# Performance work log

Hardware: AMD Instinct MI355X
Metric: run time of the kernel (lower is better)

The kernel has to match this reference:

```python
import jax, jax.numpy as jnp
import numpy as np
from jax import lax

SEQ_LEN = 4096
INPUT_SIZE = 1024
HIDDEN = 1024
NUM_CLASSES = 3


def setup_inputs() -> dict:
    key = jax.random.key(0)
    ks = jax.random.split(key, 12)
    s = 1.0 / np.sqrt(HIDDEN)  # torch LSTM/Linear uniform init scale
    def u(k, shape):
        return jax.random.uniform(k, shape, jnp.float32, -s, s)
    inp = jax.random.normal(ks[0], (SEQ_LEN, 1, INPUT_SIZE), jnp.float32)
    return {
        "inp": inp,
        # forward-direction LSTM params (gate order i,f,g,o as in torch)
        "Wih_f": u(ks[1], (4 * HIDDEN, INPUT_SIZE)),
        "Whh_f": u(ks[2], (4 * HIDDEN, HIDDEN)),
        "bih_f": u(ks[3], (4 * HIDDEN,)),
        "bhh_f": u(ks[4], (4 * HIDDEN,)),
        # backward-direction LSTM params
        "Wih_b": u(ks[5], (4 * HIDDEN, INPUT_SIZE)),
        "Whh_b": u(ks[6], (4 * HIDDEN, HIDDEN)),
        "bih_b": u(ks[7], (4 * HIDDEN,)),
        "bhh_b": u(ks[8], (4 * HIDDEN,)),
        # output head: Linear(2*HIDDEN, 3)
        "W_ho": u(ks[9], (NUM_CLASSES, 2 * HIDDEN)),
        "b_ho": u(ks[10], (NUM_CLASSES,)),
    }


def _lstm_last_h(x, Wih, Whh, bih, bhh):
    # x: (T, B, I) -> final hidden state (B, H)
    H = Whh.shape[1]
    B = x.shape[1]
    bias = bih + bhh
    # precompute input projections for all timesteps: (T, B, 4H)
    xg = jnp.einsum('tbi,gi->tbg', x, Wih) + bias

    def step(carry, xt):
        h, c = carry
        gates = xt + h @ Whh.T  # (B, 4H)
        i, f, g, o = jnp.split(gates, 4, axis=-1)
        c = jax.nn.sigmoid(f) * c + jax.nn.sigmoid(i) * jnp.tanh(g)
        h = jax.nn.sigmoid(o) * jnp.tanh(c)
        return (h, c), None

    init = (jnp.zeros((B, H), x.dtype), jnp.zeros((B, H), x.dtype))
    (hT, _), _ = lax.scan(step, init, xg)
    return hT


def reference(inp, Wih_f, Whh_f, bih_f, bhh_f, Wih_b, Whh_b, bih_b, bhh_b, W_ho, b_ho):
    h_fwd = _lstm_last_h(inp, Wih_f, Whh_f, bih_f, bhh_f)          # (1, H)
    h_bwd = _lstm_last_h(inp[::-1], Wih_b, Whh_b, bih_b, bhh_b)    # (1, H)
    hidden = jnp.concatenate([h_fwd, h_bwd], axis=-1)              # (1, 2H)
    # Dropout(p=0.35) is identity in eval mode.
    return hidden @ W_ho.T + b_ho                                  # (1, 3)
```

## Files before the change

kernel.cpp:

```cpp
#include <hip/hip_runtime.h>
#include <stdint.h>
#include <math.h>


#define T_SEQ 4096
#define ISZ   1024
#define HID   1024
#define NB_DIR 128
#define NB_TOT 256
#define NTHR   512
#define ROWS_PER_BLK 32
#define UNITS_PER_BLK 8
#define KW 64
#define PAD_CHUNK 68

typedef unsigned long long u64;

__device__ __forceinline__ float fast_sigmoid(float x) {
    return 1.0f / (1.0f + __expf(-x));
}
__device__ __forceinline__ float fast_tanh(float x) {
    return 1.0f - 2.0f / (__expf(2.0f * x) + 1.0f);
}

__global__ __launch_bounds__(NTHR, 2)
void bilstm_persistent(const float* __restrict__ x,
                       const float* __restrict__ Wih_f, const float* __restrict__ Whh_f,
                       const float* __restrict__ bih_f, const float* __restrict__ bhh_f,
                       const float* __restrict__ Wih_b, const float* __restrict__ Whh_b,
                       const float* __restrict__ bih_b, const float* __restrict__ bhh_b,
                       u64* hpack )
{
    const int tid = threadIdx.x;
    const int blk = blockIdx.x;
    const int dir = blk >> 7;
    const int lb  = blk & 127;
    const int u0  = lb * UNITS_PER_BLK;
    const int r_local = tid >> 4;
    const int kc  = tid & 15;
    const int q   = r_local >> 3;
    const int uu  = r_local & 7;
    const int grow = q * HID + u0 + uu;

    const float* Wih = dir ? Wih_b : Wih_f;
    const float* Whh = dir ? Whh_b : Whh_f;
    const float* bih = dir ? bih_b : bih_f;
    const float* bhh = dir ? bhh_b : bhh_f;

    u64* hp = hpack + (size_t)dir * 2 * HID;

    __shared__ float lds_h[16 * PAD_CHUNK];
    __shared__ float lds_x[16 * PAD_CHUNK];
    __shared__ float lds_g[ROWS_PER_BLK];
    __shared__ float lds_bias[ROWS_PER_BLK];

    float wih[KW], whh[KW];
    {
        const float* pih = Wih + (size_t)grow * ISZ + kc * KW;
        const float* phh = Whh + (size_t)grow * HID + kc * KW;
        #pragma unroll
        for (int j = 0; j < KW; j += 4) {
            float4 a = *(const float4*)(pih + j);
            wih[j] = a.x; wih[j+1] = a.y; wih[j+2] = a.z; wih[j+3] = a.w;
            float4 b4 = *(const float4*)(phh + j);
            whh[j] = b4.x; whh[j+1] = b4.y; whh[j+2] = b4.z; whh[j+3] = b4.w;
        }
    }
    #pragma unroll
    for (int j = 0; j < KW; ++j) {
        asm volatile("" : "+v"(wih[j]));
        asm volatile("" : "+v"(whh[j]));
    }

    if (tid < ROWS_PER_BLK) {
        int qq = tid >> 3, u2 = tid & 7;
        int gr = qq * HID + u0 + u2;
        lds_bias[tid] = bih[gr] + bhh[gr];
    }

    float c_state = 0.0f;

    {
        int xrow = dir ? (T_SEQ - 1) : 0;
        const float* xp = x + (size_t)xrow * ISZ;
        int i0 = tid * 2;
        float2 v = *(const float2*)(xp + i0);
        *(float2*)&lds_x[(i0 >> 6) * PAD_CHUNK + (i0 & 63)] = v;
    }
    __syncthreads();
    float xacc = 0.0f;
    {
        const float* lx = lds_x + kc * PAD_CHUNK;
        #pragma unroll
        for (int j = 0; j < KW; j += 4) {
            float4 v = *(const float4*)(lx + j);
            xacc += wih[j]*v.x + wih[j+1]*v.y + wih[j+2]*v.z + wih[j+3]*v.w;
        }
    }

    bool dead = false;

    for (int t = 0; t < T_SEQ; ++t) {
        float pre = xacc;

        if (t > 0) {
            u64* src = hp + ((size_t)((t - 1) & 1)) * HID;
            const int pi = tid * 2;
            u64 e0 = 0, e1 = 0;
            if (!dead) {
                int sp = 0;
                while (((e0 = __hip_atomic_load(src + pi, __ATOMIC_RELAXED,
                                                __HIP_MEMORY_SCOPE_AGENT)) >> 32)
                       != (unsigned)t) {
                    if (++sp > (1 << 21)) { dead = true; break; }
                }
                sp = 0;
                if (!dead) {
                    while (((e1 = __hip_atomic_load(src + pi + 1, __ATOMIC_RELAXED,
                                                    __HIP_MEMORY_SCOPE_AGENT)) >> 32)
                           != (unsigned)t) {
                        if (++sp > (1 << 21)) { dead = true; break; }
                    }
                }
            }
            lds_h[(pi >> 6) * PAD_CHUNK + (pi & 63)] =
                __uint_as_float((unsigned)(e0 & 0xffffffffu));
            lds_h[((pi + 1) >> 6) * PAD_CHUNK + ((pi + 1) & 63)] =
                __uint_as_float((unsigned)(e1 & 0xffffffffu));
            __syncthreads();
            const float* lh = lds_h + kc * PAD_CHUNK;
            #pragma unroll
            for (int j = 0; j < KW; j += 4) {
                float4 v = *(const float4*)(lh + j);
                pre += whh[j]*v.x + whh[j+1]*v.y + whh[j+2]*v.z + whh[j+3]*v.w;
            }
        }

        pre += __shfl_xor(pre, 1);
        pre += __shfl_xor(pre, 2);
        pre += __shfl_xor(pre, 4);
        pre += __shfl_xor(pre, 8);
        if (kc == 0) lds_g[r_local] = pre + lds_bias[r_local];
        __syncthreads();

        if (tid < UNITS_PER_BLK) {
            float gi = lds_g[0 * 8 + tid];
            float gf = lds_g[1 * 8 + tid];
            float gg = lds_g[2 * 8 + tid];
            float go = lds_g[3 * 8 + tid];
            float si = fast_sigmoid(gi);
            float sf = fast_sigmoid(gf);
            float so = fast_sigmoid(go);
            float tg = fast_tanh(gg);
            c_state = sf * c_state + si * tg;
            float hval = so * fast_tanh(c_state);
            u64 pk = ((u64)(unsigned)(t + 1) << 32) | (u64)__float_as_uint(hval);
            __hip_atomic_store(hp + ((size_t)(t & 1)) * HID + u0 + tid, pk,
                               __ATOMIC_RELAXED, __HIP_MEMORY_SCOPE_AGENT);
        }

        if (t + 1 < T_SEQ) {
            int xrow = dir ? (T_SEQ - 2 - t) : (t + 1);
            const float* xp = x + (size_t)xrow * ISZ;
            int i0 = tid * 2;
            float2 v = *(const float2*)(xp + i0);
            *(float2*)&lds_x[(i0 >> 6) * PAD_CHUNK + (i0 & 63)] = v;
            __syncthreads();
            xacc = 0.0f;
            const float* lx = lds_x + kc * PAD_CHUNK;
            #pragma unroll
            for (int j = 0; j < KW; j += 4) {
                float4 v4 = *(const float4*)(lx + j);
                xacc += wih[j]*v4.x + wih[j+1]*v4.y + wih[j+2]*v4.z + wih[j+3]*v4.w;
            }
        }
    }
}

__global__ void head_kernel(const float* __restrict__ W_ho,
                            const float* __restrict__ b_ho,
                            const u64* __restrict__ hpack,
                            float* __restrict__ out)
{
    const u64* hf  = hpack + 1 * HID;
    const u64* hbk = hpack + 2 * HID + 1 * HID;
    __shared__ float r0[4], r1[4], r2[4];
    int tid = threadIdx.x;
    float p0 = 0.f, p1 = 0.f, p2 = 0.f;
    for (int i = tid; i < 2 * HID; i += 256) {
        u64 e = (i < HID) ? hf[i] : hbk[i - HID];
        float hv = __uint_as_float((unsigned)(e & 0xffffffffu));
        p0 += W_ho[0 * 2 * HID + i] * hv;
        p1 += W_ho[1 * 2 * HID + i] * hv;
        p2 += W_ho[2 * 2 * HID + i] * hv;
    }
    #pragma unroll
    for (int m = 1; m < 64; m <<= 1) {
        p0 += __shfl_xor(p0, m);
        p1 += __shfl_xor(p1, m);
        p2 += __shfl_xor(p2, m);
    }
    int w = tid >> 6;
    if ((tid & 63) == 0) { r0[w] = p0; r1[w] = p1; r2[w] = p2; }
    __syncthreads();
    if (tid == 0) {
        out[0] = b_ho[0] + r0[0] + r0[1] + r0[2] + r0[3];
        out[1] = b_ho[1] + r1[0] + r1[1] + r1[2] + r1[3];
        out[2] = b_ho[2] + r2[0] + r2[1] + r2[2] + r2[3];
    }
}

extern "C" void kernel_launch(void* const* d_in, const int* in_sizes, int n_in,
                              void* d_out, int out_size, void* d_ws, size_t ws_size,
                              hipStream_t stream) {
    const float* x     = (const float*)d_in[0];
    const float* Wih_f = (const float*)d_in[1];
    const float* Whh_f = (const float*)d_in[2];
    const float* bih_f = (const float*)d_in[3];
    const float* bhh_f = (const float*)d_in[4];
    const float* Wih_b = (const float*)d_in[5];
    const float* Whh_b = (const float*)d_in[6];
    const float* bih_b = (const float*)d_in[7];
    const float* bhh_b = (const float*)d_in[8];
    const float* W_ho  = (const float*)d_in[9];
    const float* b_ho  = (const float*)d_in[10];

    u64* hpack = (u64*)d_ws;

    hipMemsetAsync(d_ws, 0, 2 * 2 * HID * sizeof(u64), stream);

    bilstm_persistent<<<NB_TOT, NTHR, 0, stream>>>(
        x, Wih_f, Whh_f, bih_f, bhh_f, Wih_b, Whh_b, bih_b, bhh_b, hpack);

    head_kernel<<<1, 256, 0, stream>>>(W_ho, b_ho, hpack, (float*)d_out);
}
```

Measured before the change: 8.955 ms.

## Hoist input projection into a separate GEMM and slim the recurrent step

Computes the input projections for all timesteps and both directions up front with a tiled FP32 GEMM into workspace, as the reference does, so the persistent recurrent kernel keeps only Whh in registers. Each wavefront now owns one hidden unit, and the four gates are gathered with lane shuffles instead of an LDS round trip. This drops one __syncthreads per step, and the LDS h buffer is double-buffered. The cost is an extra 128MB workspace buffer plus the write and reread traffic for it. The old fused kernel is kept as a fallback when the workspace is too small.

```diff
diff --git a/kernel.cpp b/kernel.cpp
--- a/kernel.cpp
+++ b/kernel.cpp
@@ -1,18 +1,15 @@
 #include <hip/hip_runtime.h>
 #include <stdint.h>
-#include <math.h>
 
 
 #define T_SEQ 4096
 #define ISZ   1024
 #define HID   1024
+#define G4H   4096
 #define NB_DIR 128
 #define NB_TOT 256
-#define NTHR   512
-#define ROWS_PER_BLK 32
-#define UNITS_PER_BLK 8
-#define KW 64
-#define PAD_CHUNK 68
+#define NTHR  512
+#define PAD   68
 
 typedef unsigned long long u64;
 
@@ -23,88 +20,124 @@
     return 1.0f - 2.0f / (__expf(2.0f * x) + 1.0f);
 }
 
+#define GM 64
+#define GN 64
+#define GK 32
+
+__global__ __launch_bounds__(256)
+void xproj_gemm(const float* __restrict__ x,
+                const float* __restrict__ Wih_f, const float* __restrict__ bih_f,
+                const float* __restrict__ bhh_f,
+                const float* __restrict__ Wih_b, const float* __restrict__ bih_b,
+                const float* __restrict__ bhh_b,
+                float* __restrict__ xg)
+{
+    const int dir = blockIdx.z;
+    const float* Wih = dir ? Wih_b : Wih_f;
+    const float* bih = dir ? bih_b : bih_f;
+    const float* bhh = dir ? bhh_b : bhh_f;
+    const int m0 = blockIdx.y * GM;
+    const int n0 = blockIdx.x * GN;
+    const int tid = threadIdx.x;
+    const int ms = tid >> 2;
+    const int kq = tid & 3;
+    const int tm = tid >> 4;
+    const int tn = tid & 15;
+
+    __shared__ float As[GK][GM + 4];
+    __shared__ float Bs[GK][GN + 4];
+
+    float acc[4][4] = {};
+
+    const int mrow = m0 + ms;
+    const int xrow = dir ? (T_SEQ - 1 - mrow) : mrow;
+    const float* ap = x + (size_t)xrow * ISZ + kq * 8;
+    const float* bp = Wih + (size_t)(n0 + ms) * ISZ + kq * 8;
+
+    for (int k0 = 0; k0 < ISZ; k0 += GK) {
+        float4 a0 = *(const float4*)(ap + k0);
+        float4 a1 = *(const float4*)(ap + k0 + 4);
+        float4 b0 = *(const float4*)(bp + k0);
+        float4 b1 = *(const float4*)(bp + k0 + 4);
+        __syncthreads();
+        const int kb = kq * 8;
+        As[kb+0][ms]=a0.x; As[kb+1][ms]=a0.y; As[kb+2][ms]=a0.z; As[kb+3][ms]=a0.w;
+        As[kb+4][ms]=a1.x; As[kb+5][ms]=a1.y; As[kb+6][ms]=a1.z; As[kb+7][ms]=a1.w;
+        Bs[kb+0][ms]=b0.x; Bs[kb+1][ms]=b0.y; Bs[kb+2][ms]=b0.z; Bs[kb+3][ms]=b0.w;
+        Bs[kb+4][ms]=b1.x; Bs[kb+5][ms]=b1.y; Bs[kb+6][ms]=b1.z; Bs[kb+7][ms]=b1.w;
+        __syncthreads();
+        #pragma unroll
+        for (int k = 0; k < GK; ++k) {
+            float4 av = *(const float4*)&As[k][tm * 4];
+            float4 bv = *(const float4*)&Bs[k][tn * 4];
+            acc[0][0] += av.x*bv.x; acc[0][1] += av.x*bv.y; acc[0][2] += av.x*bv.z; acc[0][3] += av.x*bv.w;
+            acc[1][0] += av.y*bv.x; acc[1][1] += av.y*bv.y; acc[1][2] += av.y*bv.z; acc[1][3] += av.y*bv.w;
+            acc[2][0] += av.z*bv.x; acc[2][1] += av.z*bv.y; acc[2][2] += av.z*bv.z; acc[2][3] += av.z*bv.w;
+            acc[3][0] += av.w*bv.x; acc[3][1] += av.w*bv.y; acc[3][2] += av.w*bv.z; acc[3][3] += av.w*bv.w;
+        }
+    }
+
+    const int gc = n0 + tn * 4;
+    float4 bb1 = *(const float4*)(bih + gc);
+    float4 bb2 = *(const float4*)(bhh + gc);
+    float bx = bb1.x + bb2.x, by = bb1.y + bb2.y, bz = bb1.z + bb2.z, bw = bb1.w + bb2.w;
+    float* op = xg + ((size_t)dir << 24) + (size_t)(m0 + tm * 4) * G4H + gc;
+    #pragma unroll
+    for (int i = 0; i < 4; ++i) {
+        float4 v;
+        v.x = acc[i][0] + bx; v.y = acc[i][1] + by;
+        v.z = acc[i][2] + bz; v.w = acc[i][3] + bw;
+        *(float4*)(op + (size_t)i * G4H) = v;
+    }
+}
+
 __global__ __launch_bounds__(NTHR, 2)
-void bilstm_persistent(const float* __restrict__ x,
-                       const float* __restrict__ Wih_f, const float* __restrict__ Whh_f,
-                       const float* __restrict__ bih_f, const float* __restrict__ bhh_f,
-                       const float* __restrict__ Wih_b, const float* __restrict__ Whh_b,
-                       const float* __restrict__ bih_b, const float* __restrict__ bhh_b,
-                       u64* hpack )
+void bilstm_rec(const float* __restrict__ xg,
+                const float* __restrict__ Whh_f, const float* __restrict__ Whh_b,
+                u64* hpack)
 {
     const int tid = threadIdx.x;
     const int blk = blockIdx.x;
     const int dir = blk >> 7;
     const int lb  = blk & 127;
-    const int u0  = lb * UNITS_PER_BLK;
-    const int r_local = tid >> 4;
-    const int kc  = tid & 15;
-    const int q   = r_local >> 3;
-    const int uu  = r_local & 7;
-    const int grow = q * HID + u0 + uu;
-
-    const float* Wih = dir ? Wih_b : Wih_f;
+    const int u0  = lb * 8;
+    const int w   = tid >> 6;
+    const int lane = tid & 63;
+    const int q   = lane >> 4;
+    const int kc  = lane & 15;
+    const int grow = q * HID + u0 + w;
+
     const float* Whh = dir ? Whh_b : Whh_f;
-    const float* bih = dir ? bih_b : bih_f;
-    const float* bhh = dir ? bhh_b : bhh_f;
-
+    const float* xgd = xg + ((size_t)dir << 24);
     u64* hp = hpack + (size_t)dir * 2 * HID;
 
-    __shared__ float lds_h[16 * PAD_CHUNK];
-    __shared__ float lds_x[16 * PAD_CHUNK];
-    __shared__ float lds_g[ROWS_PER_BLK];
-    __shared__ float lds_bias[ROWS_PER_BLK];
-
-    float wih[KW], whh[KW];
+    __shared__ float lds_h[2][16 * PAD];
+
+    float whh[64];
     {
-        const float* pih = Wih + (size_t)grow * ISZ + kc * KW;
-        const float* phh = Whh + (size_t)grow * HID + kc * KW;
+        const float* phh = Whh + (size_t)grow * HID + kc * 64;
         #pragma unroll
-        for (int j = 0; j < KW; j += 4) {
-            float4 a = *(const float4*)(pih + j);
-            wih[j] = a.x; wih[j+1] = a.y; wih[j+2] = a.z; wih[j+3] = a.w;
-            float4 b4 = *(const float4*)(phh + j);
-            whh[j] = b4.x; whh[j+1] = b4.y; whh[j+2] = b4.z; whh[j+3] = b4.w;
+        for (int j = 0; j < 64; j += 4) {
+            float4 v = *(const float4*)(phh + j);
+            whh[j] = v.x; whh[j+1] = v.y; whh[j+2] = v.z; whh[j+3] = v.w;
         }
     }
     #pragma unroll
-    for (int j = 0; j < KW; ++j) {
-        asm volatile("" : "+v"(wih[j]));
-        asm volatile("" : "+v"(whh[j]));
-    }
-
-    if (tid < ROWS_PER_BLK) {
-        int qq = tid >> 3, u2 = tid & 7;
-        int gr = qq * HID + u0 + u2;
-        lds_bias[tid] = bih[gr] + bhh[gr];
-    }
+    for (int j = 0; j < 64; ++j) asm volatile("" : "+v"(whh[j]));
 
     float c_state = 0.0f;
-
-    {
-        int xrow = dir ? (T_SEQ - 1) : 0;
-        const float* xp = x + (size_t)xrow * ISZ;
-        int i0 = tid * 2;
-        float2 v = *(const float2*)(xp + i0);
-        *(float2*)&lds_x[(i0 >> 6) * PAD_CHUNK + (i0 & 63)] = v;
-    }
-    __syncthreads();
-    float xacc = 0.0f;
-    {
-        const float* lx = lds_x + kc * PAD_CHUNK;
-        #pragma unroll
-        for (int j = 0; j < KW; j += 4) {
-            float4 v = *(const float4*)(lx + j);
-            xacc += wih[j]*v.x + wih[j+1]*v.y + wih[j+2]*v.z + wih[j+3]*v.w;
-        }
-    }
+    float xgv = 0.0f;
+    if (kc == 0) xgv = xgd[grow];
+    asm volatile("" : "+v"(xgv));
 
     bool dead = false;
 
     for (int t = 0; t < T_SEQ; ++t) {
-        float pre = xacc;
+        float pre = 0.0f;
 
         if (t > 0) {
-            u64* src = hp + ((size_t)((t - 1) & 1)) * HID;
+            const int b = (t - 1) & 1;
+            u64* src = hp + (size_t)b * HID;
             const int pi = tid * 2;
             u64 e0 = 0, e1 = 0;
             if (!dead) {
@@ -123,16 +156,16 @@
                     }
                 }
             }
-            lds_h[(pi >> 6) * PAD_CHUNK + (pi & 63)] =
-                __uint_as_float((unsigned)(e0 & 0xffffffffu));
-            lds_h[((pi + 1) >> 6) * PAD_CHUNK + ((pi + 1) & 63)] =
-                __uint_as_float((unsigned)(e1 & 0xffffffffu));
+            float2 hv;
+            hv.x = __uint_as_float((unsigned)(e0 & 0xffffffffu));
+            hv.y = __uint_as_float((unsigned)(e1 & 0xffffffffu));
+            *(float2*)&lds_h[b][(pi >> 6) * PAD + (pi & 63)] = hv;
             __syncthreads();
-            const float* lh = lds_h + kc * PAD_CHUNK;
+            const float* lh = &lds_h[b][kc * PAD];
             #pragma unroll
-            for (int j = 0; j < KW; j += 4) {
-                float4 v = *(const float4*)(lh + j);
-                pre += whh[j]*v.x + whh[j+1]*v.y + whh[j+2]*v.z + whh[j+3]*v.w;
+            for (int j = 0; j < 16; ++j) {
+                float4 v = *(const float4*)(lh + j * 4);
+                pre += whh[j*4+0]*v.x + whh[j*4+1]*v.y + whh[j*4+2]*v.z + whh[j*4+3]*v.w;
             }
         }
 
@@ -140,38 +173,29 @@
         pre += __shfl_xor(pre, 2);
         pre += __shfl_xor(pre, 4);
         pre += __shfl_xor(pre, 8);
-        if (kc == 0) lds_g[r_local] = pre + lds_bias[r_local];
-        __syncthreads();
-
-        if (tid < UNITS_PER_BLK) {
-            float gi = lds_g[0 * 8 + tid];
-            float gf = lds_g[1 * 8 + tid];
-            float gg = lds_g[2 * 8 + tid];
-            float go = lds_g[3 * 8 + tid];
-            float si = fast_sigmoid(gi);
-            float sf = fast_sigmoid(gf);
-            float so = fast_sigmoid(go);
-            float tg = fast_tanh(gg);
+
+        float pg = pre + xgv;
+
+        float pf_g = __shfl(pg, 16);
+        float pg_g = __shfl(pg, 32);
+        float po_g = __shfl(pg, 48);
+
+        if (lane == 0) {
+            float si = fast_sigmoid(pg);
+            float sf = fast_sigmoid(pf_g);
+            float tg = fast_tanh(pg_g);
+            float so = fast_sigmoid(po_g);
             c_state = sf * c_state + si * tg;
             float hval = so * fast_tanh(c_state);
             u64 pk = ((u64)(unsigned)(t + 1) << 32) | (u64)__float_as_uint(hval);
-            __hip_atomic_store(hp + ((size_t)(t & 1)) * HID + u0 + tid, pk,
+            __hip_atomic_store(hp + (size_t)(t & 1) * HID + u0 + w, pk,
                                __ATOMIC_RELAXED, __HIP_MEMORY_SCOPE_AGENT);
         }
 
         if (t + 1 < T_SEQ) {
-            int xrow = dir ? (T_SEQ - 2 - t) : (t + 1);
-            const float* xp = x + (size_t)xrow * ISZ;
-            int i0 = tid * 2;
-            float2 v = *(const float2*)(xp + i0);
-            *(float2*)&lds_x[(i0 >> 6) * PAD_CHUNK + (i0 & 63)] = v;
-            __syncthreads();
-            xacc = 0.0f;
-            const float* lx = lds_x + kc * PAD_CHUNK;
-            #pragma unroll
-            for (int j = 0; j < KW; j += 4) {
-                float4 v4 = *(const float4*)(lx + j);
-                xacc += wih[j]*v4.x + wih[j+1]*v4.y + wih[j+2]*v4.z + wih[j+3]*v4.w;
+            if (kc == 0) {
+                xgv = xgd[(size_t)(t + 1) * G4H + grow];
+                asm volatile("" : "+v"(xgv));
             }
         }
     }
@@ -210,6 +234,150 @@
     }
 }
 
+#define ROWS_PER_BLK 32
+#define UNITS_PER_BLK 8
+#define KW 64
+
+__global__ __launch_bounds__(NTHR, 2)
+void bilstm_fallback(const float* __restrict__ x,
+                     const float* __restrict__ Wih_f, const float* __restrict__ Whh_f,
+                     const float* __restrict__ bih_f, const float* __restrict__ bhh_f,
+                     const float* __restrict__ Wih_b, const float* __restrict__ Whh_b,
+                     const float* __restrict__ bih_b, const float* __restrict__ bhh_b,
+                     u64* hpack)
+{
+    const int tid = threadIdx.x;
+    const int blk = blockIdx.x;
+    const int dir = blk >> 7;
+    const int lb  = blk & 127;
+    const int u0  = lb * UNITS_PER_BLK;
+    const int r_local = tid >> 4;
+    const int kc  = tid & 15;
+    const int q   = r_local >> 3;
+    const int uu  = r_local & 7;
+    const int grow = q * HID + u0 + uu;
+
+    const float* Wih = dir ? Wih_b : Wih_f;
+    const float* Whh = dir ? Whh_b : Whh_f;
+    const float* bih = dir ? bih_b : bih_f;
+    const float* bhh = dir ? bhh_b : bhh_f;
+    u64* hp = hpack + (size_t)dir * 2 * HID;
+
+    __shared__ float lds_h[16 * PAD];
+    __shared__ float lds_x[16 * PAD];
+    __shared__ float lds_g[ROWS_PER_BLK];
+    __shared__ float lds_bias[ROWS_PER_BLK];
+
+    float wih[KW], whh[KW];
+    {
+        const float* pih = Wih + (size_t)grow * ISZ + kc * KW;
+        const float* phh = Whh + (size_t)grow * HID + kc * KW;
+        #pragma unroll
+        for (int j = 0; j < KW; j += 4) {
+            float4 a = *(const float4*)(pih + j);
+            wih[j] = a.x; wih[j+1] = a.y; wih[j+2] = a.z; wih[j+3] = a.w;
+            float4 b4 = *(const float4*)(phh + j);
+            whh[j] = b4.x; whh[j+1] = b4.y; whh[j+2] = b4.z; whh[j+3] = b4.w;
+        }
+    }
+    #pragma unroll
+    for (int j = 0; j < KW; ++j) {
+        asm volatile("" : "+v"(wih[j]));
+        asm volatile("" : "+v"(whh[j]));
+    }
+    if (tid < ROWS_PER_BLK) {
+        int qq = tid >> 3, u2 = tid & 7;
+        int gr = qq * HID + u0 + u2;
+        lds_bias[tid] = bih[gr] + bhh[gr];
+    }
+    float c_state = 0.0f;
+    {
+        int xrow = dir ? (T_SEQ - 1) : 0;
+        const float* xp = x + (size_t)xrow * ISZ;
+        int i0 = tid * 2;
+        float2 v = *(const float2*)(xp + i0);
+        *(float2*)&lds_x[(i0 >> 6) * PAD + (i0 & 63)] = v;
+    }
+    __syncthreads();
+    float xacc = 0.0f;
+    {
+        const float* lx = lds_x + kc * PAD;
+        #pragma unroll
+        for (int j = 0; j < KW; j += 4) {
+            float4 v = *(const float4*)(lx + j);
+            xacc += wih[j]*v.x + wih[j+1]*v.y + wih[j+2]*v.z + wih[j+3]*v.w;
+        }
+    }
+    bool dead = false;
+    for (int t = 0; t < T_SEQ; ++t) {
+        float pre = xacc;
+        if (t > 0) {
+            u64* src = hp + ((size_t)((t - 1) & 1)) * HID;
+            const int pi = tid * 2;
+            u64 e0 = 0, e1 = 0;
+            if (!dead) {
+                int sp = 0;
+                while (((e0 = __hip_atomic_load(src + pi, __ATOMIC_RELAXED,
+                                                __HIP_MEMORY_SCOPE_AGENT)) >> 32) != (unsigned)t) {
+                    if (++sp > (1 << 21)) { dead = true; break; }
+                }
+                sp = 0;
+                if (!dead) {
+                    while (((e1 = __hip_atomic_load(src + pi + 1, __ATOMIC_RELAXED,
+                                                    __HIP_MEMORY_SCOPE_AGENT)) >> 32) != (unsigned)t) {
+                        if (++sp > (1 << 21)) { dead = true; break; }
+                    }
+                }
+            }
+            lds_h[(pi >> 6) * PAD + (pi & 63)] = __uint_as_float((unsigned)(e0 & 0xffffffffu));
+            lds_h[((pi + 1) >> 6) * PAD + ((pi + 1) & 63)] = __uint_as_float((unsigned)(e1 & 0xffffffffu));
+            __syncthreads();
+            const float* lh = lds_h + kc * PAD;
+            #pragma unroll
+            for (int j = 0; j < KW; j += 4) {
+                float4 v = *(const float4*)(lh + j);
+                pre += whh[j]*v.x + whh[j+1]*v.y + whh[j+2]*v.z + whh[j+3]*v.w;
+            }
+        }
+        pre += __shfl_xor(pre, 1);
+        pre += __shfl_xor(pre, 2);
+        pre += __shfl_xor(pre, 4);
+        pre += __shfl_xor(pre, 8);
+        if (kc == 0) lds_g[r_local] = pre + lds_bias[r_local];
+        __syncthreads();
+        if (tid < UNITS_PER_BLK) {
+            float gi = lds_g[0 * 8 + tid];
+            float gf = lds_g[1 * 8 + tid];
+            float gg = lds_g[2 * 8 + tid];
+            float go = lds_g[3 * 8 + tid];
+            float si = fast_sigmoid(gi);
+            float sf = fast_sigmoid(gf);
+            float so = fast_sigmoid(go);
+            float tg = fast_tanh(gg);
+            c_state = sf * c_state + si * tg;
+            float hval = so * fast_tanh(c_state);
+            u64 pk = ((u64)(unsigned)(t + 1) << 32) | (u64)__float_as_uint(hval);
+            __hip_atomic_store(hp + ((size_t)(t & 1)) * HID + u0 + tid, pk,
+                               __ATOMIC_RELAXED, __HIP_MEMORY_SCOPE_AGENT);
+        }
+        if (t + 1 < T_SEQ) {
+            int xrow = dir ? (T_SEQ - 2 - t) : (t + 1);
+            const float* xp = x + (size_t)xrow * ISZ;
+            int i0 = tid * 2;
+            float2 v = *(const float2*)(xp + i0);
+            *(float2*)&lds_x[(i0 >> 6) * PAD + (i0 & 63)] = v;
+            __syncthreads();
+            xacc = 0.0f;
+            const float* lx = lds_x + kc * PAD;
+            #pragma unroll
+            for (int j = 0; j < KW; j += 4) {
+                float4 v4 = *(const float4*)(lx + j);
+                xacc += wih[j]*v4.x + wih[j+1]*v4.y + wih[j+2]*v4.z + wih[j+3]*v4.w;
+            }
+        }
+    }
+}
+
 extern "C" void kernel_launch(void* const* d_in, const int* in_sizes, int n_in,
                               void* d_out, int out_size, void* d_ws, size_t ws_size,
                               hipStream_t stream) {
@@ -226,11 +394,19 @@
     const float* b_ho  = (const float*)d_in[10];
 
     u64* hpack = (u64*)d_ws;
+    float* xg = (float*)((char*)d_ws + 32768);
+    const size_t need = 32768 + (size_t)2 * T_SEQ * G4H * sizeof(float);
 
     hipMemsetAsync(d_ws, 0, 2 * 2 * HID * sizeof(u64), stream);
 
-    bilstm_persistent<<<NB_TOT, NTHR, 0, stream>>>(
-        x, Wih_f, Whh_f, bih_f, bhh_f, Wih_b, Whh_b, bih_b, bhh_b, hpack);
-
+    if (ws_size >= need) {
+        dim3 gg(G4H / GN, T_SEQ / GM, 2);
+        xproj_gemm<<<gg, 256, 0, stream>>>(x, Wih_f, bih_f, bhh_f,
+                                           Wih_b, bih_b, bhh_b, xg);
+        bilstm_rec<<<NB_TOT, NTHR, 0, stream>>>(xg, Whh_f, Whh_b, hpack);
+    } else {
+        bilstm_fallback<<<NB_TOT, NTHR, 0, stream>>>(
+            x, Wih_f, Whh_f, bih_f, bhh_f, Wih_b, Whh_b, bih_b, bhh_b, hpack);
+    }
     head_kernel<<<1, 256, 0, stream>>>(W_ho, b_ho, hpack, (float*)d_out);
 }
```

Result: faster. 8.397 ms (-6.2%).

## Precompute input projections with a separate GEMM and simplify recurrent step

Applied to the files above, without the earlier changes.

Moves the per-step input projection out of the persistent recurrent kernel into a tiled FP32 GEMM that writes the gate preactivations plus bias for all timesteps to workspace. The recurrent kernel then keeps only the Whh slice in registers, gives each wavefront one hidden unit with all four gates, and reduces with wave shuffles instead of an LDS gate buffer and an extra barrier. It also double-buffers the h vector in LDS with an XOR swizzle, removing the per-step x load and second syncthreads from the serial path. In exchange it adds a large workspace (128 MB of xg) and a GEMM launch before the recurrence.

```diff
diff --git a/kernel.cpp b/kernel.cpp
--- a/kernel.cpp
+++ b/kernel.cpp
@@ -1,18 +1,12 @@
 #include <hip/hip_runtime.h>
 #include <stdint.h>
-#include <math.h>
 
 
 #define T_SEQ 4096
 #define ISZ   1024
 #define HID   1024
-#define NB_DIR 128
 #define NB_TOT 256
-#define NTHR   512
-#define ROWS_PER_BLK 32
-#define UNITS_PER_BLK 8
-#define KW 64
-#define PAD_CHUNK 68
+#define NTHR  512
 
 typedef unsigned long long u64;
 
@@ -23,156 +17,199 @@
     return 1.0f - 2.0f / (__expf(2.0f * x) + 1.0f);
 }
 
+#define PIN4(v) asm volatile("" : "+v"(v.x), "+v"(v.y), "+v"(v.z), "+v"(v.w))
+#define DOT4(a, b) ((a).x*(b).x + (a).y*(b).y + (a).z*(b).z + (a).w*(b).w)
+
+#define GM 64
+#define GN 64
+#define GK 32
+
+__global__ __launch_bounds__(256)
+void xproj_gemm(const float* __restrict__ x,
+                const float* __restrict__ Wih_f, const float* __restrict__ bih_f,
+                const float* __restrict__ bhh_f,
+                const float* __restrict__ Wih_b, const float* __restrict__ bih_b,
+                const float* __restrict__ bhh_b,
+                float* __restrict__ xg)
+{
+    const int dir = blockIdx.z;
+    const float* Wih = dir ? Wih_b : Wih_f;
+    const float* bih = dir ? bih_b : bih_f;
+    const float* bhh = dir ? bhh_b : bhh_f;
+    const int m0 = blockIdx.y * GM;
+    const int n0 = blockIdx.x * GN;
+    const int tid = threadIdx.x;
+    const int ms = tid >> 2;
+    const int kq = tid & 3;
+    const int tm = tid >> 4;
+    const int tn = tid & 15;
+
+    __shared__ float As[GK][GM + 4];
+    __shared__ float Bs[GK][GN + 4];
+
+    float acc[4][4] = {};
+
+    const int mrow = m0 + ms;
+    const int xrow = dir ? (T_SEQ - 1 - mrow) : mrow;
+    const float* ap = x + (size_t)xrow * ISZ + kq * 8;
+    const float* bp = Wih + (size_t)(n0 + ms) * ISZ + kq * 8;
+
+    for (int k0 = 0; k0 < ISZ; k0 += GK) {
+        float4 a0 = *(const float4*)(ap + k0);
+        float4 a1 = *(const float4*)(ap + k0 + 4);
+        float4 b0 = *(const float4*)(bp + k0);
+        float4 b1 = *(const float4*)(bp + k0 + 4);
+        __syncthreads();
+        const int kb = kq * 8;
+        As[kb+0][ms]=a0.x; As[kb+1][ms]=a0.y; As[kb+2][ms]=a0.z; As[kb+3][ms]=a0.w;
+        As[kb+4][ms]=a1.x; As[kb+5][ms]=a1.y; As[kb+6][ms]=a1.z; As[kb+7][ms]=a1.w;
+        Bs[kb+0][ms]=b0.x; Bs[kb+1][ms]=b0.y; Bs[kb+2][ms]=b0.z; Bs[kb+3][ms]=b0.w;
+        Bs[kb+4][ms]=b1.x; Bs[kb+5][ms]=b1.y; Bs[kb+6][ms]=b1.z; Bs[kb+7][ms]=b1.w;
+        __syncthreads();
+        #pragma unroll
+        for (int k = 0; k < GK; ++k) {
+            float4 av = *(const float4*)&As[k][tm * 4];
+            float4 bv = *(const float4*)&Bs[k][tn * 4];
+            acc[0][0] += av.x*bv.x; acc[0][1] += av.x*bv.y; acc[0][2] += av.x*bv.z; acc[0][3] += av.x*bv.w;
+            acc[1][0] += av.y*bv.x; acc[1][1] += av.y*bv.y; acc[1][2] += av.y*bv.z; acc[1][3] += av.y*bv.w;
+            acc[2][0] += av.z*bv.x; acc[2][1] += av.z*bv.y; acc[2][2] += av.z*bv.z; acc[2][3] += av.z*bv.w;
+            acc[3][0] += av.w*bv.x; acc[3][1] += av.w*bv.y; acc[3][2] += av.w*bv.z; acc[3][3] += av.w*bv.w;
+        }
+    }
+
+    const int gc = n0 + tn * 4;
+    float4 bb1 = *(const float4*)(bih + gc);
+    float4 bb2 = *(const float4*)(bhh + gc);
+    float bx = bb1.x + bb2.x, by = bb1.y + bb2.y, bz = bb1.z + bb2.z, bw = bb1.w + bb2.w;
+    float* op = xg + ((size_t)dir << 24) + (size_t)(m0 + tm * 4) * 4096 + gc;
+    #pragma unroll
+    for (int i = 0; i < 4; ++i) {
+        float4 v;
+        v.x = acc[i][0] + bx; v.y = acc[i][1] + by;
+        v.z = acc[i][2] + bz; v.w = acc[i][3] + bw;
+        *(float4*)(op + (size_t)i * 4096) = v;
+    }
+}
+
 __global__ __launch_bounds__(NTHR, 2)
-void bilstm_persistent(const float* __restrict__ x,
-                       const float* __restrict__ Wih_f, const float* __restrict__ Whh_f,
-                       const float* __restrict__ bih_f, const float* __restrict__ bhh_f,
-                       const float* __restrict__ Wih_b, const float* __restrict__ Whh_b,
-                       const float* __restrict__ bih_b, const float* __restrict__ bhh_b,
-                       u64* hpack )
+void bilstm_rec(const float* __restrict__ xg,
+                const float* __restrict__ Whh_f, const float* __restrict__ Whh_b,
+                u64* hpack)
 {
     const int tid = threadIdx.x;
     const int blk = blockIdx.x;
     const int dir = blk >> 7;
     const int lb  = blk & 127;
-    const int u0  = lb * UNITS_PER_BLK;
-    const int r_local = tid >> 4;
-    const int kc  = tid & 15;
-    const int q   = r_local >> 3;
-    const int uu  = r_local & 7;
-    const int grow = q * HID + u0 + uu;
-
-    const float* Wih = dir ? Wih_b : Wih_f;
+    const int u0  = lb * 8;
+    const int w   = tid >> 6;
+    const int l   = tid & 63;
+    const int unit = u0 + w;
+    const int xsh = ((l >> 1) & 3) << 2;
+
     const float* Whh = dir ? Whh_b : Whh_f;
-    const float* bih = dir ? bih_b : bih_f;
-    const float* bhh = dir ? bhh_b : bhh_f;
-
+    const float* xgd = xg + ((size_t)dir << 24);
     u64* hp = hpack + (size_t)dir * 2 * HID;
 
-    __shared__ float lds_h[16 * PAD_CHUNK];
-    __shared__ float lds_x[16 * PAD_CHUNK];
-    __shared__ float lds_g[ROWS_PER_BLK];
-    __shared__ float lds_bias[ROWS_PER_BLK];
-
-    float wih[KW], whh[KW];
-    {
-        const float* pih = Wih + (size_t)grow * ISZ + kc * KW;
-        const float* phh = Whh + (size_t)grow * HID + kc * KW;
-        #pragma unroll
-        for (int j = 0; j < KW; j += 4) {
-            float4 a = *(const float4*)(pih + j);
-            wih[j] = a.x; wih[j+1] = a.y; wih[j+2] = a.z; wih[j+3] = a.w;
-            float4 b4 = *(const float4*)(phh + j);
-            whh[j] = b4.x; whh[j+1] = b4.y; whh[j+2] = b4.z; whh[j+3] = b4.w;
-        }
-    }
-    #pragma unroll
-    for (int j = 0; j < KW; ++j) {
-        asm volatile("" : "+v"(wih[j]));
-        asm volatile("" : "+v"(whh[j]));
-    }
-
-    if (tid < ROWS_PER_BLK) {
-        int qq = tid >> 3, u2 = tid & 7;
-        int gr = qq * HID + u0 + u2;
-        lds_bias[tid] = bih[gr] + bhh[gr];
-    }
+    __shared__ __align__(16) float lds_h[2][HID];
+
+    const float* wp0 = Whh + (size_t)(0 * HID + unit) * HID + l * 16;
+    const float* wp1 = Whh + (size_t)(1 * HID + unit) * HID + l * 16;
+    const float* wp2 = Whh + (size_t)(2 * HID + unit) * HID + l * 16;
+    const float* wp3 = Whh + (size_t)(3 * HID + unit) * HID + l * 16;
+    float4 w00 = *(const float4*)(wp0 + 0),  w01 = *(const float4*)(wp0 + 4);
+    float4 w02 = *(const float4*)(wp0 + 8),  w03 = *(const float4*)(wp0 + 12);
+    float4 w10 = *(const float4*)(wp1 + 0),  w11 = *(const float4*)(wp1 + 4);
+    float4 w12 = *(const float4*)(wp1 + 8),  w13 = *(const float4*)(wp1 + 12);
+    float4 w20 = *(const float4*)(wp2 + 0),  w21 = *(const float4*)(wp2 + 4);
+    float4 w22 = *(const float4*)(wp2 + 8),  w23 = *(const float4*)(wp2 + 12);
+    float4 w30 = *(const float4*)(wp3 + 0),  w31 = *(const float4*)(wp3 + 4);
+    float4 w32 = *(const float4*)(wp3 + 8),  w33 = *(const float4*)(wp3 + 12);
+    PIN4(w00); PIN4(w01); PIN4(w02); PIN4(w03);
+    PIN4(w10); PIN4(w11); PIN4(w12); PIN4(w13);
+    PIN4(w20); PIN4(w21); PIN4(w22); PIN4(w23);
+    PIN4(w30); PIN4(w31); PIN4(w32); PIN4(w33);
 
     float c_state = 0.0f;
-
-    {
-        int xrow = dir ? (T_SEQ - 1) : 0;
-        const float* xp = x + (size_t)xrow * ISZ;
-        int i0 = tid * 2;
-        float2 v = *(const float2*)(xp + i0);
-        *(float2*)&lds_x[(i0 >> 6) * PAD_CHUNK + (i0 & 63)] = v;
-    }
-    __syncthreads();
-    float xacc = 0.0f;
-    {
-        const float* lx = lds_x + kc * PAD_CHUNK;
-        #pragma unroll
-        for (int j = 0; j < KW; j += 4) {
-            float4 v = *(const float4*)(lx + j);
-            xacc += wih[j]*v.x + wih[j+1]*v.y + wih[j+2]*v.z + wih[j+3]*v.w;
-        }
-    }
+    float xgv = 0.0f;
+    if (l < 4) xgv = xgd[(size_t)l * HID + unit];
+    asm volatile("" : "+v"(xgv));
 
     bool dead = false;
 
     for (int t = 0; t < T_SEQ; ++t) {
-        float pre = xacc;
+        float s0 = 0.f, s1 = 0.f, s2 = 0.f, s3 = 0.f;
 
         if (t > 0) {
-            u64* src = hp + ((size_t)((t - 1) & 1)) * HID;
-            const int pi = tid * 2;
+            const int b = (t - 1) & 1;
+            u64* src = hp + (size_t)b * HID;
+            const int k0 = tid * 2;
             u64 e0 = 0, e1 = 0;
             if (!dead) {
                 int sp = 0;
-                while (((e0 = __hip_atomic_load(src + pi, __ATOMIC_RELAXED,
+                while (((e0 = __hip_atomic_load(src + k0, __ATOMIC_RELAXED,
                                                 __HIP_MEMORY_SCOPE_AGENT)) >> 32)
                        != (unsigned)t) {
                     if (++sp > (1 << 21)) { dead = true; break; }
                 }
                 sp = 0;
                 if (!dead) {
-                    while (((e1 = __hip_atomic_load(src + pi + 1, __ATOMIC_RELAXED,
+                    while (((e1 = __hip_atomic_load(src + k0 + 1, __ATOMIC_RELAXED,
                                                     __HIP_MEMORY_SCOPE_AGENT)) >> 32)
                            != (unsigned)t) {
                         if (++sp > (1 << 21)) { dead = true; break; }
                     }
                 }
             }
-            lds_h[(pi >> 6) * PAD_CHUNK + (pi & 63)] =
-                __uint_as_float((unsigned)(e0 & 0xffffffffu));
-            lds_h[((pi + 1) >> 6) * PAD_CHUNK + ((pi + 1) & 63)] =
-                __uint_as_float((unsigned)(e1 & 0xffffffffu));
+            const int mi = (k0 & ~15) | ((k0 & 15) ^ (((k0 >> 5) & 3) << 2));
+            float2 hv;
+            hv.x = __uint_as_float((unsigned)(e0 & 0xffffffffu));
+            hv.y = __uint_as_float((unsigned)(e1 & 0xffffffffu));
+            *(float2*)&lds_h[b][mi] = hv;
             __syncthreads();
-            const float* lh = lds_h + kc * PAD_CHUNK;
-            #pragma unroll
-            for (int j = 0; j < KW; j += 4) {
-                float4 v = *(const float4*)(lh + j);
-                pre += whh[j]*v.x + whh[j+1]*v.y + whh[j+2]*v.z + whh[j+3]*v.w;
-            }
-        }
-
-        pre += __shfl_xor(pre, 1);
-        pre += __shfl_xor(pre, 2);
-        pre += __shfl_xor(pre, 4);
-        pre += __shfl_xor(pre, 8);
-        if (kc == 0) lds_g[r_local] = pre + lds_bias[r_local];
-        __syncthreads();
-
-        if (tid < UNITS_PER_BLK) {
-            float gi = lds_g[0 * 8 + tid];
-            float gf = lds_g[1 * 8 + tid];
-            float gg = lds_g[2 * 8 + tid];
-            float go = lds_g[3 * 8 + tid];
+
+            const float* lh = &lds_h[b][l * 16];
+            float4 h0 = *(const float4*)(lh + (0  ^ xsh));
+            float4 h1 = *(const float4*)(lh + (4  ^ xsh));
+            float4 h2 = *(const float4*)(lh + (8  ^ xsh));
+            float4 h3 = *(const float4*)(lh + (12 ^ xsh));
+
+            s0 = DOT4(w00,h0) + DOT4(w01,h1) + DOT4(w02,h2) + DOT4(w03,h3);
+            s1 = DOT4(w10,h0) + DOT4(w11,h1) + DOT4(w12,h2) + DOT4(w13,h3);
+            s2 = DOT4(w20,h0) + DOT4(w21,h1) + DOT4(w22,h2) + DOT4(w23,h3);
+            s3 = DOT4(w30,h0) + DOT4(w31,h1) + DOT4(w32,h2) + DOT4(w33,h3);
+        }
+
+        #pragma unroll
+        for (int m = 1; m < 64; m <<= 1) {
+            s0 += __shfl_xor(s0, m);
+            s1 += __shfl_xor(s1, m);
+            s2 += __shfl_xor(s2, m);
+            s3 += __shfl_xor(s3, m);
+        }
+
+        float xg1 = __shfl(xgv, 1);
+        float xg2 = __shfl(xgv, 2);
+        float xg3 = __shfl(xgv, 3);
+
+        if (l == 0) {
+            float gi = s0 + xgv;
+            float gf = s1 + xg1;
+            float gg = s2 + xg2;
+            float go = s3 + xg3;
             float si = fast_sigmoid(gi);
             float sf = fast_sigmoid(gf);
+            float tg = fast_tanh(gg);
             float so = fast_sigmoid(go);
-            float tg = fast_tanh(gg);
             c_state = sf * c_state + si * tg;
             float hval = so * fast_tanh(c_state);
             u64 pk = ((u64)(unsigned)(t + 1) << 32) | (u64)__float_as_uint(hval);
-            __hip_atomic_store(hp + ((size_t)(t & 1)) * HID + u0 + tid, pk,
+            __hip_atomic_store(hp + (size_t)(t & 1) * HID + unit, pk,
                                __ATOMIC_RELAXED, __HIP_MEMORY_SCOPE_AGENT);
         }
 
-        if (t + 1 < T_SEQ) {
-            int xrow = dir ? (T_SEQ - 2 - t) : (t + 1);
-            const float* xp = x + (size_t)xrow * ISZ;
-            int i0 = tid * 2;
-            float2 v = *(const float2*)(xp + i0);
-            *(float2*)&lds_x[(i0 >> 6) * PAD_CHUNK + (i0 & 63)] = v;
-            __syncthreads();
-            xacc = 0.0f;
-            const float* lx = lds_x + kc * PAD_CHUNK;
-            #pragma unroll
-            for (int j = 0; j < KW; j += 4) {
-                float4 v4 = *(const float4*)(lx + j);
-                xacc += wih[j]*v4.x + wih[j+1]*v4.y + wih[j+2]*v4.z + wih[j+3]*v4.w;
-            }
+        if (t + 1 < T_SEQ && l < 4) {
+            xgv = xgd[(size_t)(t + 1) * 4096 + (size_t)l * HID + unit];
+            asm volatile("" : "+v"(xgv));
         }
     }
 }
@@ -226,11 +263,13 @@
     const float* b_ho  = (const float*)d_in[10];
 
     u64* hpack = (u64*)d_ws;
+    float* xg = (float*)((char*)d_ws + 32768);
 
     hipMemsetAsync(d_ws, 0, 2 * 2 * HID * sizeof(u64), stream);
 
-    bilstm_persistent<<<NB_TOT, NTHR, 0, stream>>>(
-        x, Wih_f, Whh_f, bih_f, bhh_f, Wih_b, Whh_b, bih_b, bhh_b, hpack);
-
+    dim3 gg(4096 / GN, T_SEQ / GM, 2);
+    xproj_gemm<<<gg, 256, 0, stream>>>(x, Wih_f, bih_f, bhh_f,
+                                       Wih_b, bih_b, bhh_b, xg);
+    bilstm_rec<<<NB_TOT, NTHR, 0, stream>>>(xg, Whh_f, Whh_b, hpack);
     head_kernel<<<1, 256, 0, stream>>>(W_ho, b_ho, hpack, (float*)d_out);
 }
```

After: 9.291 ms. 3.7% more time.
